# Kernel tuning notes

Hardware: AMD Instinct MI355X
Metric: run time of the kernel (lower is better)

Reference implementation:

```python
import jax, jax.numpy as jnp
import numpy as np

B, L, T = 512, 2048, 16
START_TAG, STOP_TAG = 0, 1


def setup_inputs() -> dict:
    key = jax.random.key(0)
    k1, k2, k3, k4 = jax.random.split(key, 4)
    feats = jax.random.normal(k1, (B, L, T), dtype=jnp.float32)
    # contiguous prefix masks (the torch code assumes valid tokens come first:
    # _score_sentence indexes tags[b, mask.sum()] as the last gold tag)
    lengths = jax.random.randint(k2, (B,), L // 2, L + 1)
    mask = (jnp.arange(L)[None, :] < lengths[:, None]).astype(jnp.int32)
    tgt = jax.random.randint(k3, (B, L), 2, T)  # gold tags, avoid START/STOP ids
    transitions = jax.random.normal(k4, (T, T), dtype=jnp.float32)
    return {"feats": feats, "mask": mask, "tgt": tgt, "transitions": transitions}


def _forward_alg(feats_tm, mask_tm, transitions):
    """CRF partition function. feats_tm: [L,B,T] time-major, mask_tm: [L,B] bool."""
    Bn, Tn = feats_tm.shape[1], feats_tm.shape[2]
    init = jnp.full((Bn, Tn), -10000.0, dtype=feats_tm.dtype).at[:, START_TAG].set(0.0)

    def step(fv, inp):
        feat_t, m_t = inp  # feat_t: [B,T], m_t: [B]
        # scores[b, next, prev] = fv[b, prev] + transitions[next, prev]
        scores = fv[:, None, :] + transitions[None, :, :]
        alphas = jax.nn.logsumexp(scores, axis=-1) + feat_t  # [B,T]
        fv_new = jnp.where(m_t[:, None], alphas, fv)  # freeze padded positions
        return fv_new, None

    fv, _ = jax.lax.scan(step, init, (feats_tm, mask_tm))
    terminal = fv + transitions[STOP_TAG][None, :]  # [B,T]
    return jax.nn.logsumexp(terminal, axis=-1)  # [B]


def _score_sentence(feats, mask, tgt, transitions):
    """Gold path score. feats: [B,L,T], mask: [B,L] int, tgt: [B,L] int."""
    Bn = feats.shape[0]
    tags = jnp.concatenate(
        [jnp.full((Bn, 1), START_TAG, dtype=tgt.dtype), tgt], axis=1)  # [B,L+1]
    cur, prev = tags[:, 1:], tags[:, :-1]  # each [B,L]
    trans_sc = transitions[cur, prev]  # [B,L]
    emit_sc = jnp.take_along_axis(feats, cur[:, :, None], axis=2)[:, :, 0]  # [B,L]
    fmask = mask.astype(feats.dtype)
    score = jnp.sum((trans_sc + emit_sc) * fmask, axis=1)  # [B]
    lengths = mask.sum(axis=1)  # [B]
    last_tag = tags[jnp.arange(Bn), lengths]  # last valid gold tag
    return score + transitions[STOP_TAG, last_tag]


def reference(feats, mask, tgt, transitions):
    # Extractor.forward: mean over batch of (log Z - gold path score)
    feats_tm = jnp.transpose(feats, (1, 0, 2))  # [L,B,T]
    mask_tm = jnp.transpose(mask, (1, 0)).astype(bool)  # [L,B]
    fwd_score = _forward_alg(feats_tm, mask_tm, transitions)
    gold_score = _score_sentence(feats, mask, tgt, transitions)
    return (fwd_score - gold_score).sum() / feats.shape[0]
```

## Files before the change

### kernel.cpp

```cpp
#include <hip/hip_runtime.h>
#include <hip/hip_bf16.h>

#define Bn 512
#define Ln 2048
#define Tn 16

typedef float f32x4 __attribute__((ext_vector_type(4)));
typedef short s16x4 __attribute__((ext_vector_type(4)));
typedef int   i32x2 __attribute__((ext_vector_type(2)));

#define L2E 1.4426950408889634f
#define LN2 0.6931471805599453f

#if __has_builtin(__builtin_amdgcn_mfma_f32_16x16x16bf16_1k)
#define HAVE_MFMA1K 1
#endif

__device__ __forceinline__ f32x4 mfma16(s16x4 a, s16x4 b, f32x4 c) {
#ifdef HAVE_MFMA1K
  return __builtin_amdgcn_mfma_f32_16x16x16bf16_1k(a, b, c, 0, 0, 0);
#else
  f32x4 d;
  asm volatile("v_mfma_f32_16x16x16_bf16 %0, %1, %2, %3\n\ts_nop 7\n\ts_nop 7"
               : "=&v"(d) : "v"(a), "v"(b), "v"(c));
  return d;
#endif
}

__device__ __forceinline__ int cvtpk_bf16(float a, float b) {
  int r;
  asm("v_cvt_pk_bf16_f32 %0, %1, %2" : "=v"(r) : "v"(a), "v"(b));
  return r;
}

__device__ __forceinline__ s16x4 pack_bf16(f32x4 q) {
  i32x2 t2; t2.x = cvtpk_bf16(q.x, q.y); t2.y = cvtpk_bf16(q.z, q.w);
  return __builtin_bit_cast(s16x4, t2);
}

__device__ __forceinline__ float rl0(float x) {
  return __builtin_bit_cast(float, __builtin_amdgcn_readfirstlane(__builtin_bit_cast(int, x)));
}

#define STEPNP(fr)                                                            \
  {                                                                           \
    const float F0 = __builtin_amdgcn_exp2f(__builtin_fmaf(fr.x, L2E, mpend));\
    const float F1 = __builtin_amdgcn_exp2f(__builtin_fmaf(fr.y, L2E, mpend));\
    const float F2 = __builtin_amdgcn_exp2f(__builtin_fmaf(fr.z, L2E, mpend));\
    const float F3 = __builtin_amdgcn_exp2f(__builtin_fmaf(fr.w, L2E, mpend));\
    const f32x4 p = mfma16(afrag, bfrag, zero);                               \
    q.x = p.x * F0; q.y = p.y * F1; q.z = p.z * F2; q.w = p.w * F3;           \
    bfrag = pack_bf16(q);                                                     \
    lnacc += pend;                                                            \
    const float c0 = fmaxf(rl0(q.x), 1e-30f);                                 \
    pend = __builtin_amdgcn_logf(c0);                               \
    mpend = -pend;                                                            \
  }

#define PSTEP(fr, tt)                                                         \
  {                                                                           \
    const bool live = (tt) < nsteps;                                          \
    const float F0 = __builtin_amdgcn_exp2f(__builtin_fmaf(fr.x, L2E, mpend));\
    const float F1 = __builtin_amdgcn_exp2f(__builtin_fmaf(fr.y, L2E, mpend));\
    const float F2 = __builtin_amdgcn_exp2f(__builtin_fmaf(fr.z, L2E, mpend));\
    const float F3 = __builtin_amdgcn_exp2f(__builtin_fmaf(fr.w, L2E, mpend));\
    const f32x4 p = mfma16(afrag, bfrag, zero);                               \
    f32x4 qn;                                                                 \
    qn.x = p.x * F0; qn.y = p.y * F1; qn.z = p.z * F2; qn.w = p.w * F3;       \
    const float c0n = fmaxf(rl0(qn.x), 1e-30f);                               \
    if (live) {                                                               \
      q = qn; bfrag = pack_bf16(qn);                                          \
      lnacc += pend;                                                          \
      pend = __builtin_amdgcn_logf(c0n);                                      \
      mpend = -pend;                                                          \
    }                                                                         \
  }

#define LOADQ(dst, ii)                                                        \
  dst = *(const float4*)(fp + (size_t)((ii) < CHrt ? (ii) : CHrt - 1) * Tn);

__global__ __launch_bounds__(256, 8) void crf_chunk(
    const float* __restrict__ feats, const int* __restrict__ mask,
    const int* __restrict__ tgt, const float* __restrict__ trans,
    float* __restrict__ wsT, float* __restrict__ wsLn, float* __restrict__ wsGold,
    int ncs)
{
  const int lane = threadIdx.x & 63;
  const int gwid = (blockIdx.x << 2) + (threadIdx.x >> 6);
  const int b = gwid >> ncs;
  const int c = gwid & ((1 << ncs) - 1);
  const int CHrt = Ln >> ncs;
  const int col = lane & 15;
  const int r0 = (lane >> 4) << 2;

  s16x4 afrag;
  {
    const float4 tr = *(const float4*)(trans + col * 16 + r0);
    f32x4 e;
    e.x = __builtin_amdgcn_exp2f(tr.x * L2E);
    e.y = __builtin_amdgcn_exp2f(tr.y * L2E);
    e.z = __builtin_amdgcn_exp2f(tr.z * L2E);
    e.w = __builtin_amdgcn_exp2f(tr.w * L2E);
    afrag = pack_bf16(e);
  }

  const size_t bL = (size_t)b * Ln;
  const int t0 = c * CHrt;

  int nsteps;
  {
    int cnt = 0;
    if (lane * 4 < CHrt) {
      const int4 mv = *(const int4*)(mask + bL + t0 + lane * 4);
      cnt = mv.x + mv.y + mv.z + mv.w;
    }
    for (int m = 1; m < 64; m <<= 1) cnt += __shfl_xor(cnt, m);
    nsteps = cnt;
  }

  f32x4 q;
  q.x = (r0 + 0 == col) ? 1.f : 0.f;
  q.y = (r0 + 1 == col) ? 1.f : 0.f;
  q.z = (r0 + 2 == col) ? 1.f : 0.f;
  q.w = (r0 + 3 == col) ? 1.f : 0.f;
  s16x4 bfrag = pack_bf16(q);
  float lnacc = 0.f;
  const f32x4 zero = {0.f, 0.f, 0.f, 0.f};

  if (nsteps > 0) {
    const float* fp = feats + (bL + (size_t)t0) * Tn + r0;
    float pend = 0.f, mpend = 0.f;

    float4 a0, a1, a2, a3, b0, b1, b2, b3;
    LOADQ(a0, 0) LOADQ(a1, 1) LOADQ(a2, 2) LOADQ(a3, 3)

    const int full8 = nsteps >> 3;
    const int tail = nsteps & 7;
    for (int it = 0; it < full8; ++it) {
      const int base = it << 3;
      LOADQ(b0, base + 4) LOADQ(b1, base + 5) LOADQ(b2, base + 6) LOADQ(b3, base + 7)
      STEPNP(a0) STEPNP(a1) STEPNP(a2) STEPNP(a3)
      LOADQ(a0, base + 8) LOADQ(a1, base + 9) LOADQ(a2, base + 10) LOADQ(a3, base + 11)
      STEPNP(b0) STEPNP(b1) STEPNP(b2) STEPNP(b3)
    }
    if (tail) {
      const int base = full8 << 3;
      LOADQ(b0, base + 4) LOADQ(b1, base + 5) LOADQ(b2, base + 6) LOADQ(b3, base + 7)
      PSTEP(a0, base + 0) PSTEP(a1, base + 1) PSTEP(a2, base + 2) PSTEP(a3, base + 3)
      PSTEP(b0, base + 4) PSTEP(b1, base + 5) PSTEP(b2, base + 6) PSTEP(b3, base + 7)
    }
  }

  *(f32x4*)(wsT + ((size_t)gwid * 64 + lane) * 4) = q;
  if (lane == 0) wsLn[gwid] = lnacc;

  float gs = 0.f;
  const int ngold = CHrt >> 6;
  for (int k2 = 0; k2 < ngold; ++k2) {
    const int t = t0 + k2 * 64 + lane;
    if (mask[bL + t]) {
      const int cur = tgt[bL + t];
      const int prv = (t == 0) ? 0 : tgt[bL + t - 1];
      gs += trans[cur * 16 + prv] + feats[(bL + t) * 16 + cur];
    }
  }
  for (int m = 1; m < 64; m <<= 1) gs += __shfl_xor(gs, m);
  if (lane == 0) atomicAdd(wsGold + b, gs);
}

__global__ __launch_bounds__(256) void crf_combine(
    const int* __restrict__ mask, const int* __restrict__ tgt,
    const float* __restrict__ trans, const float* __restrict__ wsT,
    const float* __restrict__ wsLn, const float* __restrict__ wsGold,
    float* __restrict__ out, int ncs)
{
  const int lane = threadIdx.x & 63;
  const int b = (blockIdx.x << 2) + (threadIdx.x >> 6);
  const int col = lane & 15;
  const int NCrt = 1 << ncs;

  float u = (col == 0) ? 1.f : 0.f;
  float Lacc = 0.f;

  for (int c = 0; c < NCrt; ++c) {
    const float4 tf = *(const float4*)(wsT + (((size_t)(b << ncs) + c) * 64 + lane) * 4);
    float p0 = tf.x * u, p1 = tf.y * u, p2 = tf.z * u, p3 = tf.w * u;
    for (int m = 1; m < 16; m <<= 1) {
      p0 += __shfl_xor(p0, m); p1 += __shfl_xor(p1, m);
      p2 += __shfl_xor(p2, m); p3 += __shfl_xor(p3, m);
    }
    const float pre = (lane & 2) ? ((lane & 1) ? p3 : p2) : ((lane & 1) ? p1 : p0);
    const int srcl = ((lane & 12) << 2) + (lane & 3);
    float un = __shfl(pre, srcl);
    const float c0 = fmaxf(rl0(un), 1e-30f);
    Lacc += __builtin_amdgcn_logf(c0) + wsLn[(size_t)(b << ncs) + c];
    u = un * __builtin_amdgcn_rcpf(c0);
  }

  float v = u * __builtin_amdgcn_exp2f(trans[16 + col] * L2E);
  for (int m = 1; m < 16; m <<= 1) v += __shfl_xor(v, m);
  v = fmaxf(v, 1e-30f);
  const float fwd = LN2 * (Lacc + __builtin_amdgcn_logf(v));

  const size_t bL = (size_t)b * Ln;
  int cnt = 0;
  for (int i = lane; i < Ln; i += 64) cnt += mask[bL + i];
  for (int m = 1; m < 64; m <<= 1) cnt += __shfl_xor(cnt, m);

  if (lane == 0) {
    const int last = tgt[bL + cnt - 1];
    const float gold = wsGold[b] + trans[16 + last];
    atomicAdd(out, (fwd - gold) * (1.f / 512.f));
  }
}

extern "C" void kernel_launch(void* const* d_in, const int* in_sizes, int n_in,
                              void* d_out, int out_size, void* d_ws, size_t ws_size,
                              hipStream_t stream) {
  const float* feats = (const float*)d_in[0];
  const int* mask = (const int*)d_in[1];
  const int* tgt = (const int*)d_in[2];
  const float* trans = (const float*)d_in[3];
  float* out = (float*)d_out;

  char* ws = (char*)d_ws;
  float* wsGold = (float*)ws;
  float* wsLn   = (float*)(ws + 2048);
  float* wsT    = (float*)(ws + 2048 + 32768);

  const size_t need16 = 2048 + 32768 + (size_t)16 * Bn * 256 * 4;
  const int ncs = (ws_size >= need16) ? 4 : 3;
  const int nwaves = Bn << ncs;

  hipMemsetAsync(d_out, 0, sizeof(float), stream);
  hipMemsetAsync(wsGold, 0, Bn * sizeof(float), stream);

  crf_chunk<<<nwaves / 4, 256, 0, stream>>>(feats, mask, tgt, trans, wsT, wsLn, wsGold, ncs);
  crf_combine<<<Bn / 4, 256, 0, stream>>>(mask, tgt, trans, wsT, wsLn, wsGold, out, ncs);
}
```

Baseline: 87.91 us.

## Balance CRF chunks by valid length and share exp across lanes

Adds a prepass kernel that computes per-sequence valid lengths, so each chunk wave now splits only the valid prefix evenly instead of fixed time windows. Padded sequences therefore no longer leave some waves idle while others run the full serial chain. The inner loop now does one coalesced exp per lane per 4 timesteps and broadcasts the factors with shuffles, instead of four exps per lane per step. Renormalisation runs every other step, with a reciprocal scale folded in, rather than every step. The cost is an extra kernel launch and looser renorm, which risks overflow in the bf16/fp32 range, while the combine kernel reuses the stored lengths.

```diff
diff --git a/kernel.cpp b/kernel.cpp
--- a/kernel.cpp
+++ b/kernel.cpp
@@ -42,46 +42,50 @@
   return __builtin_bit_cast(float, __builtin_amdgcn_readfirstlane(__builtin_bit_cast(int, x)));
 }
 
-#define STEPNP(fr)                                                            \
+__global__ __launch_bounds__(256) void len_kernel(const int* __restrict__ mask,
+                                                  int* __restrict__ wsLen) {
+  const int lane = threadIdx.x & 63;
+  const int b = (blockIdx.x << 2) + (threadIdx.x >> 6);
+  const int4* mp = (const int4*)(mask + (size_t)b * Ln);
+  int cnt = 0;
+#pragma unroll
+  for (int i = 0; i < Ln / 4 / 64; ++i) {
+    int4 v = mp[i * 64 + lane];
+    cnt += v.x + v.y + v.z + v.w;
+  }
+  for (int m = 1; m < 64; m <<= 1) cnt += __shfl_xor(cnt, m);
+  if (lane == 0) wsLen[b] = cnt;
+}
+
+#define GBODY(j, APPLY, RENORM)                                               \
   {                                                                           \
-    const float F0 = __builtin_amdgcn_exp2f(__builtin_fmaf(fr.x, L2E, mpend));\
-    const float F1 = __builtin_amdgcn_exp2f(__builtin_fmaf(fr.y, L2E, mpend));\
-    const float F2 = __builtin_amdgcn_exp2f(__builtin_fmaf(fr.z, L2E, mpend));\
-    const float F3 = __builtin_amdgcn_exp2f(__builtin_fmaf(fr.w, L2E, mpend));\
+    float F0 = __shfl(exCur, ((j) << 4) + r0 + 0);                            \
+    float F1 = __shfl(exCur, ((j) << 4) + r0 + 1);                            \
+    float F2 = __shfl(exCur, ((j) << 4) + r0 + 2);                            \
+    float F3 = __shfl(exCur, ((j) << 4) + r0 + 3);                            \
     const f32x4 p = mfma16(afrag, bfrag, zero);                               \
+    if (APPLY) { F0 *= s; F1 *= s; F2 *= s; F3 *= s; lnacc += pend; }         \
     q.x = p.x * F0; q.y = p.y * F1; q.z = p.z * F2; q.w = p.w * F3;           \
     bfrag = pack_bf16(q);                                                     \
-    lnacc += pend;                                                            \
-    const float c0 = fmaxf(rl0(q.x), 1e-30f);                                 \
-    pend = __builtin_amdgcn_logf(c0);                               \
-    mpend = -pend;                                                            \
-  }
-
-#define PSTEP(fr, tt)                                                         \
-  {                                                                           \
-    const bool live = (tt) < nsteps;                                          \
-    const float F0 = __builtin_amdgcn_exp2f(__builtin_fmaf(fr.x, L2E, mpend));\
-    const float F1 = __builtin_amdgcn_exp2f(__builtin_fmaf(fr.y, L2E, mpend));\
-    const float F2 = __builtin_amdgcn_exp2f(__builtin_fmaf(fr.z, L2E, mpend));\
-    const float F3 = __builtin_amdgcn_exp2f(__builtin_fmaf(fr.w, L2E, mpend));\
-    const f32x4 p = mfma16(afrag, bfrag, zero);                               \
-    f32x4 qn;                                                                 \
-    qn.x = p.x * F0; qn.y = p.y * F1; qn.z = p.z * F2; qn.w = p.w * F3;       \
-    const float c0n = fmaxf(rl0(qn.x), 1e-30f);                               \
-    if (live) {                                                               \
-      q = qn; bfrag = pack_bf16(qn);                                          \
-      lnacc += pend;                                                          \
-      pend = __builtin_amdgcn_logf(c0n);                                      \
-      mpend = -pend;                                                          \
+    if (RENORM) {                                                             \
+      const float c0 = fmaxf(rl0(q.x), 1e-30f);                               \
+      pend = __builtin_amdgcn_logf(c0);                             \
+      s = __builtin_amdgcn_rcpf(c0);                                          \
     }                                                                         \
   }
 
-#define LOADQ(dst, ii)                                                        \
-  dst = *(const float4*)(fp + (size_t)((ii) < CHrt ? (ii) : CHrt - 1) * Tn);
+#define GSTEP(j, APPLY, RENORM) GBODY(j, APPLY, RENORM)
+#define TSTEP(j, APPLY, RENORM)                                               \
+  if (tbase + (j) < nsteps) GBODY(j, APPLY, RENORM)
+
+#define LOADG(dst, tb)                                                        \
+  { const int tcl = min((tb) + (lane >> 4), Ln - 1);                          \
+    dst = fbase[(size_t)tcl * 16 + (lane & 15)]; }
 
 __global__ __launch_bounds__(256, 8) void crf_chunk(
     const float* __restrict__ feats, const int* __restrict__ mask,
     const int* __restrict__ tgt, const float* __restrict__ trans,
+    const int* __restrict__ wsLen,
     float* __restrict__ wsT, float* __restrict__ wsLn, float* __restrict__ wsGold,
     int ncs)
 {
@@ -89,7 +93,6 @@
   const int gwid = (blockIdx.x << 2) + (threadIdx.x >> 6);
   const int b = gwid >> ncs;
   const int c = gwid & ((1 << ncs) - 1);
-  const int CHrt = Ln >> ncs;
   const int col = lane & 15;
   const int r0 = (lane >> 4) << 2;
 
@@ -105,18 +108,10 @@
   }
 
   const size_t bL = (size_t)b * Ln;
-  const int t0 = c * CHrt;
-
-  int nsteps;
-  {
-    int cnt = 0;
-    if (lane * 4 < CHrt) {
-      const int4 mv = *(const int4*)(mask + bL + t0 + lane * 4);
-      cnt = mv.x + mv.y + mv.z + mv.w;
-    }
-    for (int m = 1; m < 64; m <<= 1) cnt += __shfl_xor(cnt, m);
-    nsteps = cnt;
-  }
+  const int len = wsLen[b];
+  const int t0s = (c * len) >> ncs;
+  const int t1s = ((c + 1) * len) >> ncs;
+  const int nsteps = t1s - t0s;
 
   f32x4 q;
   q.x = (r0 + 0 == col) ? 1.f : 0.f;
@@ -124,30 +119,26 @@
   q.z = (r0 + 2 == col) ? 1.f : 0.f;
   q.w = (r0 + 3 == col) ? 1.f : 0.f;
   s16x4 bfrag = pack_bf16(q);
-  float lnacc = 0.f;
+  float lnacc = 0.f, s = 1.f, pend = 0.f;
   const f32x4 zero = {0.f, 0.f, 0.f, 0.f};
 
-  if (nsteps > 0) {
-    const float* fp = feats + (bL + (size_t)t0) * Tn + r0;
-    float pend = 0.f, mpend = 0.f;
-
-    float4 a0, a1, a2, a3, b0, b1, b2, b3;
-    LOADQ(a0, 0) LOADQ(a1, 1) LOADQ(a2, 2) LOADQ(a3, 3)
-
-    const int full8 = nsteps >> 3;
-    const int tail = nsteps & 7;
-    for (int it = 0; it < full8; ++it) {
-      const int base = it << 3;
-      LOADQ(b0, base + 4) LOADQ(b1, base + 5) LOADQ(b2, base + 6) LOADQ(b3, base + 7)
-      STEPNP(a0) STEPNP(a1) STEPNP(a2) STEPNP(a3)
-      LOADQ(a0, base + 8) LOADQ(a1, base + 9) LOADQ(a2, base + 10) LOADQ(a3, base + 11)
-      STEPNP(b0) STEPNP(b1) STEPNP(b2) STEPNP(b3)
+  {
+    const float* fbase = feats + bL * 16;
+    float fvN, exCur, exNext;
+    { float fv0; LOADG(fv0, t0s); exCur = __builtin_amdgcn_exp2f(fv0 * L2E); }
+    LOADG(fvN, t0s + 4);
+
+    const int nfull = nsteps >> 2;
+    const int tail = nsteps & 3;
+    for (int g = 0; g < nfull; ++g) {
+      exNext = __builtin_amdgcn_exp2f(fvN * L2E);
+      LOADG(fvN, t0s + (g + 2) * 4);
+      GSTEP(0, 1, 0) GSTEP(1, 0, 1) GSTEP(2, 1, 0) GSTEP(3, 0, 1)
+      exCur = exNext;
     }
     if (tail) {
-      const int base = full8 << 3;
-      LOADQ(b0, base + 4) LOADQ(b1, base + 5) LOADQ(b2, base + 6) LOADQ(b3, base + 7)
-      PSTEP(a0, base + 0) PSTEP(a1, base + 1) PSTEP(a2, base + 2) PSTEP(a3, base + 3)
-      PSTEP(b0, base + 4) PSTEP(b1, base + 5) PSTEP(b2, base + 6) PSTEP(b3, base + 7)
+      const int tbase = nfull << 2;
+      TSTEP(0, 1, 0) TSTEP(1, 0, 1) TSTEP(2, 1, 0)
     }
   }
 
@@ -155,9 +146,11 @@
   if (lane == 0) wsLn[gwid] = lnacc;
 
   float gs = 0.f;
+  const int CHrt = Ln >> ncs;
+  const int tg0 = c * CHrt;
   const int ngold = CHrt >> 6;
   for (int k2 = 0; k2 < ngold; ++k2) {
-    const int t = t0 + k2 * 64 + lane;
+    const int t = tg0 + k2 * 64 + lane;
     if (mask[bL + t]) {
       const int cur = tgt[bL + t];
       const int prv = (t == 0) ? 0 : tgt[bL + t - 1];
@@ -169,8 +162,8 @@
 }
 
 __global__ __launch_bounds__(256) void crf_combine(
-    const int* __restrict__ mask, const int* __restrict__ tgt,
-    const float* __restrict__ trans, const float* __restrict__ wsT,
+    const int* __restrict__ tgt, const float* __restrict__ trans,
+    const int* __restrict__ wsLen, const float* __restrict__ wsT,
     const float* __restrict__ wsLn, const float* __restrict__ wsGold,
     float* __restrict__ out, int ncs)
 {
@@ -202,13 +195,10 @@
   v = fmaxf(v, 1e-30f);
   const float fwd = LN2 * (Lacc + __builtin_amdgcn_logf(v));
 
-  const size_t bL = (size_t)b * Ln;
-  int cnt = 0;
-  for (int i = lane; i < Ln; i += 64) cnt += mask[bL + i];
-  for (int m = 1; m < 64; m <<= 1) cnt += __shfl_xor(cnt, m);
-
   if (lane == 0) {
-    const int last = tgt[bL + cnt - 1];
+    const size_t bL = (size_t)b * Ln;
+    const int len = wsLen[b];
+    const int last = tgt[bL + len - 1];
     const float gold = wsGold[b] + trans[16 + last];
     atomicAdd(out, (fwd - gold) * (1.f / 512.f));
   }
@@ -224,17 +214,20 @@
   float* out = (float*)d_out;
 
   char* ws = (char*)d_ws;
-  float* wsGold = (float*)ws;
-  float* wsLn   = (float*)(ws + 2048);
-  float* wsT    = (float*)(ws + 2048 + 32768);
-
-  const size_t need16 = 2048 + 32768 + (size_t)16 * Bn * 256 * 4;
+  int*   wsLen  = (int*)ws;
+  float* wsGold = (float*)(ws + 2048);
+  float* wsLn   = (float*)(ws + 4096);
+  float* wsT    = (float*)(ws + 4096 + 32768);
+
+  const size_t need16 = 4096 + 32768 + (size_t)16 * Bn * 256 * 4;
   const int ncs = (ws_size >= need16) ? 4 : 3;
   const int nwaves = Bn << ncs;
 
   hipMemsetAsync(d_out, 0, sizeof(float), stream);
   hipMemsetAsync(wsGold, 0, Bn * sizeof(float), stream);
 
-  crf_chunk<<<nwaves / 4, 256, 0, stream>>>(feats, mask, tgt, trans, wsT, wsLn, wsGold, ncs);
-  crf_combine<<<Bn / 4, 256, 0, stream>>>(mask, tgt, trans, wsT, wsLn, wsGold, out, ncs);
-}
+  len_kernel<<<Bn / 4, 256, 0, stream>>>(mask, wsLen);
+  crf_chunk<<<nwaves / 4, 256, 0, stream>>>(feats, mask, tgt, trans, wsLen,
+                                            wsT, wsLn, wsGold, ncs);
+  crf_combine<<<Bn / 4, 256, 0, stream>>>(tgt, trans, wsLen, wsT, wsLn, wsGold, out, ncs);
+}
```

Measured after the change: 73.09 us. -16.9%, faster.
